# Performance work log

Measured on AMD Instinct MI355X. Metric: run time of the kernel, lower is better.

The kernel has to match this reference:

```python
import jax, jax.numpy as jnp
import numpy as np

EPS = 1e-6

def setup_inputs() -> dict:
    key = jax.random.key(0)
    ks = jax.random.split(key, 9)
    B, T, D = 4, 1024, 128
    sc = 1.0 / np.sqrt(D)
    return {
        "x_seq": jax.random.normal(ks[0], (B, T, D), dtype=jnp.float32),
        "Wq": jax.random.uniform(ks[1], (D, D), jnp.float32, -sc, sc),
        "bq": jax.random.uniform(ks[2], (D,), jnp.float32, -sc, sc),
        "Wk": jax.random.uniform(ks[3], (D, D), jnp.float32, -sc, sc),
        "bk": jax.random.uniform(ks[4], (D,), jnp.float32, -sc, sc),
        "Wv": jax.random.uniform(ks[5], (D, D), jnp.float32, -sc, sc),
        "bv": jax.random.uniform(ks[6], (D,), jnp.float32, -sc, sc),
        "Wa": jax.random.uniform(ks[7], (D, D), jnp.float32, -sc, sc),
        "ba": jax.random.uniform(ks[8], (D,), jnp.float32, -sc, sc),
    }

def reference(x_seq, Wq, bq, Wk, bk, Wv, bv, Wa, ba):
    B, T, D = x_seq.shape
    q = jax.nn.relu(x_seq @ Wq.T + bq)          # [B,T,D]
    k = jax.nn.relu(x_seq @ Wk.T + bk)
    v = x_seq @ Wv.T + bv
    A = jax.nn.sigmoid(x_seq @ Wa.T + ba)       # per-step decay gate

    def step(carry, inp):
        s, z = carry                             # s:[B,D,D], z:[B,D]
        a_t, k_t, v_t, q_t = inp                 # each [B,D]
        s = a_t[:, :, None] * s + k_t[:, :, None] * v_t[:, None, :]  # s[b,i,j]=a_i*s + k_i v_j
        z = a_t * z + k_t
        num = jnp.einsum('bi,bij->bj', q_t, s)
        den = jnp.sum(q_t * z, axis=-1, keepdims=True) + EPS
        return (s, z), num / den

    s0 = jnp.zeros((B, D, D), x_seq.dtype)
    z0 = jnp.zeros((B, D), x_seq.dtype)
    xs = (jnp.swapaxes(A, 0, 1), jnp.swapaxes(k, 0, 1),
          jnp.swapaxes(v, 0, 1), jnp.swapaxes(q, 0, 1))  # time-major [T,B,D]
    _, y = jax.lax.scan(step, (s0, z0), xs)
    return jnp.swapaxes(y, 0, 1)                 # [B,T,D]
```

## Files before the change

kernel.cpp:

```cpp
#include <hip/hip_runtime.h>

#define BB 4
#define TT 1024
#define DD 128
#define LL 16
#define CC 64
#define EPSV 1e-6f

#define OFF_QC   0
#define OFF_KH   (OFF_QC + BB*TT*DD)
#define OFF_V    (OFF_KH + BB*TT*DD)
#define OFF_CL   (OFF_V  + BB*TT*DD)
#define OFF_KS   (OFF_CL + BB*CC*DD)
#define OFF_Z0   (OFF_KS + BB*CC*DD)
#define OFF_U    (OFF_Z0 + BB*CC*DD)
#define OFF_S0   (OFF_U  + BB*CC*DD*DD)
#define OFF_G    (OFF_S0 + BB*CC*DD*DD)

__global__ __launch_bounds__(256) void k_gemm(
    const float* __restrict__ x,
    const float* __restrict__ Wq, const float* __restrict__ bq,
    const float* __restrict__ Wk, const float* __restrict__ bk,
    const float* __restrict__ Wv, const float* __restrict__ bv,
    const float* __restrict__ Wa, const float* __restrict__ ba,
    float* __restrict__ ws)
{
    __shared__ float xs [32][DD];
    __shared__ float wsh[64][132];

    const int tid = threadIdx.x;
    const int bx  = blockIdx.x;
    const int rt  = bx >> 3;
    const int mt  = bx & 7;
    const int m   = mt >> 1;
    const int jh  = mt & 1;

    const float* W    = (m==0)?Wq : (m==1)?Wk : (m==2)?Wv : Wa;
    const float* bias = (m==0)?bq : (m==1)?bk : (m==2)?bv : ba;

    {
        const float4* xg = (const float4*)(x + (size_t)rt*32*DD);
        #pragma unroll
        for (int r=0;r<4;r++){
            int f = tid + r*256;
            *(float4*)&xs[f>>5][(f&31)*4] = xg[f];
        }
        const float4* wg = (const float4*)(W + (size_t)jh*64*DD);
        #pragma unroll
        for (int r=0;r<8;r++){
            int f = tid + r*256;
            *(float4*)&wsh[f>>5][(f&31)*4] = wg[f];
        }
    }
    __syncthreads();

    const int ci = tid & 15;
    const int ri = tid >> 4;

    float acc[2][4];
    #pragma unroll
    for (int cc=0;cc<4;cc++){
        float bv_ = bias[jh*64 + ci + 16*cc];
        acc[0][cc]=bv_; acc[1][cc]=bv_;
    }

    #pragma unroll 2
    for (int k4=0; k4<32; k4++){
        float4 xa = *(const float4*)&xs[ri   ][k4*4];
        float4 xb = *(const float4*)&xs[ri+16][k4*4];
        #pragma unroll
        for (int cc=0;cc<4;cc++){
            float4 w = *(const float4*)&wsh[ci+16*cc][k4*4];
            acc[0][cc] = fmaf(xa.x,w.x, fmaf(xa.y,w.y, fmaf(xa.z,w.z, fmaf(xa.w,w.w, acc[0][cc]))));
            acc[1][cc] = fmaf(xb.x,w.x, fmaf(xb.y,w.y, fmaf(xb.z,w.z, fmaf(xb.w,w.w, acc[1][cc]))));
        }
    }

    float* dst = ws + ((m==0)?OFF_QC : (m==1)?OFF_KH : (m==2)?OFF_V : OFF_G);
    #pragma unroll
    for (int rr=0;rr<2;rr++){
        int row = rt*32 + ri + 16*rr;
        #pragma unroll
        for (int cc=0;cc<4;cc++){
            float v = acc[rr][cc];
            if (m==0 || m==1) v = fmaxf(v, 0.f);
            else if (m==3)    v = 1.f/(1.f+__expf(-v));
            dst[(size_t)row*DD + jh*64 + ci + 16*cc] = v;
        }
    }
}

__global__ __launch_bounds__(256) void k_chunk(float* __restrict__ ws)
{
    __shared__ float ksm[LL][DD];
    __shared__ float gs [LL][DD];
    __shared__ float kbs[LL][DD];
    __shared__ float qs [LL][32];
    __shared__ float vs [LL][32];

    const int tid = threadIdx.x;
    const int bq_ = blockIdx.x;
    const int bc  = bq_ >> 2;
    const int jq  = bq_ & 3;
    const int jbase = jq * 32;
    const int b   = bc / CC;
    const int t0  = (bc % CC) * LL;
    const size_t tile = (size_t)(b*TT + t0)*DD;

    {
        const float4* kg = (const float4*)(ws + OFF_KH + tile);
        const float4* gg = (const float4*)(ws + OFF_G  + tile);
        #pragma unroll
        for (int r=0;r<2;r++){
            int f = tid + r*256;
            int t = f >> 5, c4 = (f & 31)*4;
            *(float4*)&ksm[t][c4] = kg[f];
            *(float4*)&gs [t][c4] = gg[f];
        }
        int f  = tid & 127;
        int t  = f >> 3, c = (f & 7)*4;
        const float* src = (tid < 128) ? (ws + OFF_QC) : (ws + OFF_V);
        float4 v4 = *(const float4*)(src + tile + (size_t)t*DD + jbase + c);
        if (tid < 128) *(float4*)&qs[t][c] = v4;
        else           *(float4*)&vs[t][c] = v4;
    }
    __syncthreads();

    if (tid < DD){
        float c = 1.f;
        #pragma unroll
        for (int t=0;t<LL;t++){ c *= gs[t][tid]; gs[t][tid] = c; }
        if (jq == 0) ws[OFF_CL + (size_t)bc*DD + tid] = c;
    }
    __syncthreads();

    if (tid < DD){
        const int i = tid;
        const float cl = gs[LL-1][i];
        const bool own = (i >= jbase) && (i < jbase+32);
        float ksum = 0.f;
        float* khg = ws + OFF_KH + tile;
        #pragma unroll
        for (int t=0;t<LL;t++){
            float kh = ksm[t][i] / gs[t][i];
            if (own) khg[t*DD + i] = kh;
            float kb = kh * cl;
            kbs[t][i] = kb;
            ksum += kb;
        }
        if (jq == 0) ws[OFF_KS + (size_t)bc*DD + i] = ksum;
    } else {
        const int j  = tid & 31;
        const int tg = (tid - 128) >> 5;
        float* qcg = ws + OFF_QC + tile;
        #pragma unroll
        for (int tt=0;tt<4;tt++){
            int t = tg*4 + tt;
            qcg[t*DD + jbase + j] = qs[t][j] * gs[t][jbase + j];
        }
    }
    __syncthreads();

    const int j  = tid & 31;
    const int ih = tid >> 5;
    float vr[LL];
    #pragma unroll
    for (int u=0;u<LL;u++) vr[u]=vs[u][j];
    float* Ug = ws + OFF_U + (size_t)bc*DD*DD;
    #pragma unroll
    for (int i4=0;i4<4;i4++){
        int i = ih*16 + i4*4;
        float a0=0.f,a1=0.f,a2=0.f,a3=0.f;
        #pragma unroll
        for (int u=0;u<LL;u++){
            float4 kb4 = *(const float4*)(&kbs[u][i]);
            float vu = vr[u];
            a0 = fmaf(kb4.x,vu,a0); a1 = fmaf(kb4.y,vu,a1);
            a2 = fmaf(kb4.z,vu,a2); a3 = fmaf(kb4.w,vu,a3);
        }
        Ug[(size_t)(i+0)*DD + jbase + j]=a0; Ug[(size_t)(i+1)*DD + jbase + j]=a1;
        Ug[(size_t)(i+2)*DD + jbase + j]=a2; Ug[(size_t)(i+3)*DD + jbase + j]=a3;
    }
}

__global__ __launch_bounds__(128) void k_scan(float* __restrict__ ws)
{
    __shared__ float cls[CC], kss[CC];
    const int bi = blockIdx.x;
    const int b  = bi >> 7;
    const int i  = bi & 127;
    const int j  = threadIdx.x;

    if (j < CC) cls[j]      = ws[OFF_CL + (size_t)(b*CC + j)*DD + i];
    else        kss[j - CC] = ws[OFF_KS + (size_t)(b*CC + j - CC)*DD + i];
    __syncthreads();

    const float* U  = ws + OFF_U;
    float*       s0 = ws + OFF_S0;
    float*       z0 = ws + OFF_Z0;
    const size_t base = (size_t)b*CC*DD*DD + (size_t)i*DD + j;

    float up[16];
    #pragma unroll
    for (int p=0;p<16;p++) up[p] = U[base + (size_t)p*DD*DD];

    float s = 0.f, z = 0.f;
    #pragma unroll
    for (int ch=0; ch<CC; ch++){
        s0[base + (size_t)ch*DD*DD] = s;
        if (j==0) z0[(size_t)(b*CC+ch)*DD + i] = z;
        float u  = up[ch & 15];
        if (ch + 16 < CC) up[ch & 15] = U[base + (size_t)(ch+16)*DD*DD];
        float cl = cls[ch];
        s = fmaf(cl, s, u);
        z = fmaf(cl, z, kss[ch]);
    }
}

__global__ __launch_bounds__(256) void k_out(const float* __restrict__ ws, float* __restrict__ y)
{
    __shared__ float qcs[LL][DD+4];
    __shared__ float khs[LL][DD+4];
    __shared__ float vsm[LL][64+4];
    __shared__ float Ss[LL][LL];
    __shared__ float denS[LL];
    __shared__ float z0s[DD];
    __shared__ float s0s[2][32][64+4];

    const int tid = threadIdx.x;
    const int bh  = blockIdx.x;
    const int bc  = bh >> 1;
    const int jh  = bh & 1;
    const int jbase = jh * 64;
    const int b   = bc / CC;
    const int ch  = bc % CC;
    const int t0  = ch * LL;
    const size_t tile = (size_t)(b*TT + t0)*DD;
    const float* s0g = ws + OFF_S0 + (size_t)bc*DD*DD;

    float4 pre[2];
    {
        const float4* qcg = (const float4*)(ws + OFF_QC + tile);
        const float4* khg = (const float4*)(ws + OFF_KH + tile);
        #pragma unroll
        for (int rep=0; rep<2; rep++){
            int f = tid + rep*256;
            int t = f >> 5, k4 = f & 31;
            *(float4*)&qcs[t][k4*4] = qcg[f];
            *(float4*)&khs[t][k4*4] = khg[f];
        }
        {
            int t = tid >> 4, c = (tid & 15)*4;
            *(float4*)&vsm[t][c] =
                *(const float4*)(ws + OFF_V + tile + (size_t)t*DD + jbase + c);
        }
        if (tid < DD) z0s[tid] = ws[OFF_Z0 + (size_t)bc*DD + tid];
        #pragma unroll
        for (int r=0;r<2;r++){
            int f = tid + r*256;
            int row = f >> 4, c4 = (f & 15)*4;
            pre[r] = *(const float4*)(s0g + (size_t)row*DD + jbase + c4);
        }
    }
    __syncthreads();

    {
        int t = tid >> 4, u = tid & 15;
        float s = 0.f;
        #pragma unroll 8
        for (int k4=0; k4<32; k4++){
            float4 q4 = *(const float4*)&qcs[t][k4*4];
            float4 h4 = *(const float4*)&khs[u][k4*4];
            s = fmaf(q4.x,h4.x, fmaf(q4.y,h4.y, fmaf(q4.z,h4.z, fmaf(q4.w,h4.w, s))));
        }
        Ss[t][u] = (u <= t) ? s : 0.f;
    }
    __syncthreads();

    if (tid < LL){
        int t = tid;
        float d = EPSV;
        for (int u=0; u<=t; u++) d += Ss[t][u];
        #pragma unroll 8
        for (int kk=0; kk<DD; kk++) d += qcs[t][kk]*z0s[kk];
        denS[t] = d;
    }

    const int t  = tid >> 4;
    const int jg = tid & 15;
    const int j0 = jg * 4;
    float y4[4] = {0.f,0.f,0.f,0.f};

    __syncthreads();
    #pragma unroll
    for (int u=0; u<LL; u++){
        float sv = Ss[t][u];
        float4 v4 = *(const float4*)&vsm[u][j0];
        y4[0]=fmaf(sv,v4.x,y4[0]); y4[1]=fmaf(sv,v4.y,y4[1]);
        y4[2]=fmaf(sv,v4.z,y4[2]); y4[3]=fmaf(sv,v4.w,y4[3]);
    }

    #pragma unroll
    for (int sl=0; sl<4; sl++){
        __syncthreads();
        #pragma unroll
        for (int r=0;r<2;r++){
            int f = tid + r*256;
            *(float4*)&s0s[sl&1][f>>4][(f&15)*4] = pre[r];
        }
        if (sl < 3){
            #pragma unroll
            for (int r=0;r<2;r++){
                int f = tid + r*256;
                int row = f >> 4, c4 = (f & 15)*4;
                pre[r] = *(const float4*)(s0g + (size_t)((sl+1)*32 + row)*DD + jbase + c4);
            }
        }
        __syncthreads();
        #pragma unroll 8
        for (int ii=0; ii<32; ii++){
            float qv = qcs[t][sl*32+ii];
            float4 s4 = *(const float4*)&s0s[sl&1][ii][j0];
            y4[0]=fmaf(qv,s4.x,y4[0]); y4[1]=fmaf(qv,s4.y,y4[1]);
            y4[2]=fmaf(qv,s4.z,y4[2]); y4[3]=fmaf(qv,s4.w,y4[3]);
        }
    }

    const float rd = 1.f/denS[t];
    float* yg = y + tile + (size_t)t*DD + jbase + j0;
    *(float4*)yg = make_float4(y4[0]*rd, y4[1]*rd, y4[2]*rd, y4[3]*rd);
}

extern "C" void kernel_launch(void* const* d_in, const int* in_sizes, int n_in,
                              void* d_out, int out_size, void* d_ws, size_t ws_size,
                              hipStream_t stream)
{
    const float* x  = (const float*)d_in[0];
    const float* Wq = (const float*)d_in[1]; const float* bq = (const float*)d_in[2];
    const float* Wk = (const float*)d_in[3]; const float* bk = (const float*)d_in[4];
    const float* Wv = (const float*)d_in[5]; const float* bv = (const float*)d_in[6];
    const float* Wa = (const float*)d_in[7]; const float* ba = (const float*)d_in[8];
    float* ws = (float*)d_ws;
    float* yo = (float*)d_out;

    hipLaunchKernelGGL(k_gemm,  dim3(1024),    dim3(256), 0, stream,
                       x, Wq,bq, Wk,bk, Wv,bv, Wa,ba, ws);
    hipLaunchKernelGGL(k_chunk, dim3(BB*CC*4), dim3(256), 0, stream, ws);
    hipLaunchKernelGGL(k_scan,  dim3(BB*DD),   dim3(128), 0, stream, ws);
    hipLaunchKernelGGL(k_out,   dim3(BB*CC*2), dim3(256), 0, stream, ws, yo);
}
```

Before: 117.1 us.

## Recompute per-chunk state updates in scan instead of materializing U tensor

The chunk kernel no longer writes the full per-chunk outer-product tensor U (B*C*D*D floats). It writes a transposed, decay-scaled key array instead, and the scan kernel rebuilds each U entry on the fly from that array and V using 16-term dot products. The aim is to remove a large global write and read of U, at the cost of extra FMAs and V loads inside the serial scan. The chunk kernel is also re-partitioned into two column halves per chunk with a smaller shared footprint, and the workspace layout is reordered.

```diff
diff --git a/kernel.cpp b/kernel.cpp
--- a/kernel.cpp
+++ b/kernel.cpp
@@ -7,15 +7,18 @@
 #define CC 64
 #define EPSV 1e-6f
 
+#define BTD (BB*TT*DD)
+#define BCD (BB*CC*DD)
+
 #define OFF_QC   0
-#define OFF_KH   (OFF_QC + BB*TT*DD)
-#define OFF_V    (OFF_KH + BB*TT*DD)
-#define OFF_CL   (OFF_V  + BB*TT*DD)
-#define OFF_KS   (OFF_CL + BB*CC*DD)
-#define OFF_Z0   (OFF_KS + BB*CC*DD)
-#define OFF_U    (OFF_Z0 + BB*CC*DD)
-#define OFF_S0   (OFF_U  + BB*CC*DD*DD)
-#define OFF_G    (OFF_S0 + BB*CC*DD*DD)
+#define OFF_KH   (OFF_QC + BTD)
+#define OFF_V    (OFF_KH + BTD)
+#define OFF_G    (OFF_V  + BTD)
+#define OFF_CL   (OFF_G  + BTD)
+#define OFF_KS   (OFF_CL + BCD)
+#define OFF_Z0   (OFF_KS + BCD)
+#define OFF_KBT  (OFF_Z0 + BCD)
+#define OFF_S0   (OFF_KBT + BTD)
 
 __global__ __launch_bounds__(256) void k_gemm(
     const float* __restrict__ x,
@@ -92,129 +95,125 @@
 
 __global__ __launch_bounds__(256) void k_chunk(float* __restrict__ ws)
 {
-    __shared__ float ksm[LL][DD];
-    __shared__ float gs [LL][DD];
-    __shared__ float kbs[LL][DD];
-    __shared__ float qs [LL][32];
-    __shared__ float vs [LL][32];
+    __shared__ float qs [LL][64];
+    __shared__ float krs[LL][64];
+    __shared__ float gs [LL][64];
+    __shared__ float kbs[LL][64];
 
     const int tid = threadIdx.x;
-    const int bq_ = blockIdx.x;
-    const int bc  = bq_ >> 2;
-    const int jq  = bq_ & 3;
-    const int jbase = jq * 32;
+    const int bh  = blockIdx.x;
+    const int bc  = bh >> 1;
+    const int jh  = bh & 1;
+    const int jbase = jh*64;
     const int b   = bc / CC;
     const int t0  = (bc % CC) * LL;
     const size_t tile = (size_t)(b*TT + t0)*DD;
 
     {
-        const float4* kg = (const float4*)(ws + OFF_KH + tile);
-        const float4* gg = (const float4*)(ws + OFF_G  + tile);
-        #pragma unroll
-        for (int r=0;r<2;r++){
-            int f = tid + r*256;
-            int t = f >> 5, c4 = (f & 31)*4;
-            *(float4*)&ksm[t][c4] = kg[f];
-            *(float4*)&gs [t][c4] = gg[f];
-        }
-        int f  = tid & 127;
-        int t  = f >> 3, c = (f & 7)*4;
-        const float* src = (tid < 128) ? (ws + OFF_QC) : (ws + OFF_V);
-        float4 v4 = *(const float4*)(src + tile + (size_t)t*DD + jbase + c);
-        if (tid < 128) *(float4*)&qs[t][c] = v4;
-        else           *(float4*)&vs[t][c] = v4;
-    }
-    __syncthreads();
-
-    if (tid < DD){
+        const int t = tid >> 4, c4 = (tid & 15)*4;
+        const size_t off = tile + (size_t)t*DD + jbase + c4;
+        *(float4*)&qs [t][c4] = *(const float4*)(ws + OFF_QC + off);
+        *(float4*)&krs[t][c4] = *(const float4*)(ws + OFF_KH + off);
+        *(float4*)&gs [t][c4] = *(const float4*)(ws + OFF_G  + off);
+    }
+    __syncthreads();
+
+    if (tid < 64){
         float c = 1.f;
         #pragma unroll
         for (int t=0;t<LL;t++){ c *= gs[t][tid]; gs[t][tid] = c; }
-        if (jq == 0) ws[OFF_CL + (size_t)bc*DD + tid] = c;
-    }
-    __syncthreads();
-
-    if (tid < DD){
-        const int i = tid;
-        const float cl = gs[LL-1][i];
-        const bool own = (i >= jbase) && (i < jbase+32);
-        float ksum = 0.f;
-        float* khg = ws + OFF_KH + tile;
-        #pragma unroll
-        for (int t=0;t<LL;t++){
-            float kh = ksm[t][i] / gs[t][i];
-            if (own) khg[t*DD + i] = kh;
-            float kb = kh * cl;
-            kbs[t][i] = kb;
-            ksum += kb;
-        }
-        if (jq == 0) ws[OFF_KS + (size_t)bc*DD + i] = ksum;
-    } else {
-        const int j  = tid & 31;
-        const int tg = (tid - 128) >> 5;
-        float* qcg = ws + OFF_QC + tile;
-        #pragma unroll
-        for (int tt=0;tt<4;tt++){
-            int t = tg*4 + tt;
-            qcg[t*DD + jbase + j] = qs[t][j] * gs[t][jbase + j];
-        }
-    }
-    __syncthreads();
-
-    const int j  = tid & 31;
-    const int ih = tid >> 5;
-    float vr[LL];
-    #pragma unroll
-    for (int u=0;u<LL;u++) vr[u]=vs[u][j];
-    float* Ug = ws + OFF_U + (size_t)bc*DD*DD;
-    #pragma unroll
-    for (int i4=0;i4<4;i4++){
-        int i = ih*16 + i4*4;
-        float a0=0.f,a1=0.f,a2=0.f,a3=0.f;
-        #pragma unroll
-        for (int u=0;u<LL;u++){
-            float4 kb4 = *(const float4*)(&kbs[u][i]);
-            float vu = vr[u];
-            a0 = fmaf(kb4.x,vu,a0); a1 = fmaf(kb4.y,vu,a1);
-            a2 = fmaf(kb4.z,vu,a2); a3 = fmaf(kb4.w,vu,a3);
-        }
-        Ug[(size_t)(i+0)*DD + jbase + j]=a0; Ug[(size_t)(i+1)*DD + jbase + j]=a1;
-        Ug[(size_t)(i+2)*DD + jbase + j]=a2; Ug[(size_t)(i+3)*DD + jbase + j]=a3;
+        ws[OFF_CL + (size_t)bc*DD + jbase + tid] = c;
+    }
+    __syncthreads();
+
+    {
+        const int col = tid & 63;
+        const int tg  = tid >> 6;
+        const float cl = gs[LL-1][col];
+        #pragma unroll
+        for (int r=0;r<4;r++){
+            int t = tg*4 + r;
+            float cv = gs[t][col];
+            ws[OFF_QC + tile + (size_t)t*DD + jbase + col] = qs[t][col] * cv;
+            float kh = krs[t][col] / cv;
+            ws[OFF_KH + tile + (size_t)t*DD + jbase + col] = kh;
+            kbs[t][col] = kh * cl;
+        }
+    }
+    __syncthreads();
+
+    if (tid < 64){
+        float s = 0.f;
+        #pragma unroll
+        for (int t=0;t<LL;t++) s += kbs[t][tid];
+        ws[OFF_KS + (size_t)bc*DD + jbase + tid] = s;
+    }
+    {
+        const int il = tid >> 2;
+        const int tg = tid & 3;
+        float4 v;
+        v.x = kbs[tg*4+0][il];
+        v.y = kbs[tg*4+1][il];
+        v.z = kbs[tg*4+2][il];
+        v.w = kbs[tg*4+3][il];
+        *(float4*)(ws + OFF_KBT + ((size_t)(b*DD + jbase + il)*TT + t0 + tg*4)) = v;
     }
 }
 
 __global__ __launch_bounds__(128) void k_scan(float* __restrict__ ws)
 {
+    __shared__ float kbt[TT];
     __shared__ float cls[CC], kss[CC];
+
     const int bi = blockIdx.x;
     const int b  = bi >> 7;
     const int i  = bi & 127;
     const int j  = threadIdx.x;
 
-    if (j < CC) cls[j]      = ws[OFF_CL + (size_t)(b*CC + j)*DD + i];
-    else        kss[j - CC] = ws[OFF_KS + (size_t)(b*CC + j - CC)*DD + i];
-    __syncthreads();
-
-    const float* U  = ws + OFF_U;
-    float*       s0 = ws + OFF_S0;
-    float*       z0 = ws + OFF_Z0;
-    const size_t base = (size_t)b*CC*DD*DD + (size_t)i*DD + j;
-
-    float up[16];
-    #pragma unroll
-    for (int p=0;p<16;p++) up[p] = U[base + (size_t)p*DD*DD];
+    {
+        const float4* src = (const float4*)(ws + OFF_KBT + (size_t)(b*DD + i)*TT);
+        ((float4*)kbt)[j]     = src[j];
+        ((float4*)kbt)[j+128] = src[j+128];
+        if (j < CC) cls[j]    = ws[OFF_CL + (size_t)(b*CC + j)*DD + i];
+        else        kss[j-CC] = ws[OFF_KS + (size_t)(b*CC + j-CC)*DD + i];
+    }
+    __syncthreads();
+
+    const float* Vg = ws + OFF_V + (size_t)b*TT*DD + j;
+    float* s0 = ws + OFF_S0 + (size_t)b*CC*DD*DD + (size_t)i*DD + j;
+    float* z0 = ws + OFF_Z0;
 
     float s = 0.f, z = 0.f;
-    #pragma unroll
-    for (int ch=0; ch<CC; ch++){
-        s0[base + (size_t)ch*DD*DD] = s;
-        if (j==0) z0[(size_t)(b*CC+ch)*DD + i] = z;
-        float u  = up[ch & 15];
-        if (ch + 16 < CC) up[ch & 15] = U[base + (size_t)(ch+16)*DD*DD];
-        float cl = cls[ch];
-        s = fmaf(cl, s, u);
-        z = fmaf(cl, z, kss[ch]);
-    }
+    float vA[16], vB[16];
+
+#define LOADV(dst, ch) { \
+        _Pragma("unroll") \
+        for (int u=0;u<16;u++) dst[u] = Vg[(size_t)((ch)*LL+u)*DD]; }
+
+#define STEP(vv, ch) { \
+        float p0 = kbt[(ch)*16+ 0]*vv[ 0] + kbt[(ch)*16+ 4]*vv[ 4] \
+                 + kbt[(ch)*16+ 8]*vv[ 8] + kbt[(ch)*16+12]*vv[12]; \
+        float p1 = kbt[(ch)*16+ 1]*vv[ 1] + kbt[(ch)*16+ 5]*vv[ 5] \
+                 + kbt[(ch)*16+ 9]*vv[ 9] + kbt[(ch)*16+13]*vv[13]; \
+        float p2 = kbt[(ch)*16+ 2]*vv[ 2] + kbt[(ch)*16+ 6]*vv[ 6] \
+                 + kbt[(ch)*16+10]*vv[10] + kbt[(ch)*16+14]*vv[14]; \
+        float p3 = kbt[(ch)*16+ 3]*vv[ 3] + kbt[(ch)*16+ 7]*vv[ 7] \
+                 + kbt[(ch)*16+11]*vv[11] + kbt[(ch)*16+15]*vv[15]; \
+        float Ue = (p0+p1)+(p2+p3); \
+        s0[(size_t)(ch)*DD*DD] = s; \
+        if (j==0) z0[(size_t)(b*CC+(ch))*DD + i] = z; \
+        s = fmaf(cls[ch], s, Ue); \
+        z = fmaf(cls[ch], z, kss[ch]); }
+
+    LOADV(vA, 0);
+    for (int ch=0; ch<CC; ch+=2){
+        LOADV(vB, ch+1);
+        STEP(vA, ch);
+        if (ch+2 < CC) LOADV(vA, ch+2);
+        STEP(vB, ch+1);
+    }
+#undef LOADV
+#undef STEP
 }
 
 __global__ __launch_bounds__(256) void k_out(const float* __restrict__ ws, float* __restrict__ y)
@@ -345,7 +344,7 @@
 
     hipLaunchKernelGGL(k_gemm,  dim3(1024),    dim3(256), 0, stream,
                        x, Wq,bq, Wk,bk, Wv,bv, Wa,ba, ws);
-    hipLaunchKernelGGL(k_chunk, dim3(BB*CC*4), dim3(256), 0, stream, ws);
+    hipLaunchKernelGGL(k_chunk, dim3(BB*CC*2), dim3(256), 0, stream, ws);
     hipLaunchKernelGGL(k_scan,  dim3(BB*DD),   dim3(128), 0, stream, ws);
     hipLaunchKernelGGL(k_out,   dim3(BB*CC*2), dim3(256), 0, stream, ws, yo);
 }
```

After: 128.7 us. 10.0% more time.
